# Optimization experiments

Measured on AMD Instinct MI355X. Metric: run time of the kernel, lower is better.

The kernel has to match this reference:

```python
import jax, jax.numpy as jnp
import numpy as np

H = 12          # number_of_heads
D = 768         # embedding_dim
DH = D // H     # head dim = 64
P = 14          # sqrt(num_patches) for image_size=224, patch=16
B, S = 64, 197  # batch, seq (196 patches + CLS)


def setup_inputs() -> dict:
    key = jax.random.key(0)
    ks = jax.random.split(key, 7)
    scale = 1.0 / np.sqrt(D)
    return {
        "q": jax.random.normal(ks[0], (B, S, D), jnp.float32),
        "k": jax.random.normal(ks[1], (B, S, D), jnp.float32),
        "v": jax.random.normal(ks[2], (B, S, D), jnp.float32),
        # nn.Linear weights, stored as [out, in]; applied as x @ W.T
        "Wq": jax.random.normal(ks[3], (D, D), jnp.float32) * scale,
        "Wk": jax.random.normal(ks[4], (D, D), jnp.float32) * scale,
        "Wv": jax.random.normal(ks[5], (D, D), jnp.float32) * scale,
        "Wo": jax.random.normal(ks[6], (D, D), jnp.float32) * scale,
    }


def reference(q, k, v, Wq, Wk, Wv, Wo):
    # Linear projections (bias=False): x @ W.T
    def proj(x, W):
        # [B,S,D] -> [B,H,S,DH]
        y = jnp.einsum('bsd,ed->bse', x, W)
        return y.reshape(B, S, H, DH).transpose(0, 2, 1, 3)

    qh, kh, vh = proj(q, Wq), proj(k, Wk), proj(v, Wv)

    # raw scores [B,H,S,S]
    scores = jnp.einsum('bhqd,bhkd->bhqk', qh, kh) / jnp.sqrt(jnp.asarray(DH, qh.dtype))
    attn = jax.nn.softmax(scores, axis=-1)

    # CLS (row 0) attention to the 196 patches -> [B,H,P,P]
    cls_to_patch_map = attn[:, :, 0, 1:].reshape(B, H, P, P)

    # dropout in eval mode (identity; deterministic reference)
    x = jnp.einsum('bhqk,bhkd->bhqd', attn, vh)          # [B,H,S,DH]
    x = x.transpose(0, 2, 1, 3).reshape(B, S, D)          # [B,S,D]
    output = jnp.einsum('bsd,ed->bse', x, Wo)
    return output, cls_to_patch_map
```

## Files before the change

### kernel.cpp

```cpp
#include <hip/hip_runtime.h>
#include <hip/hip_bf16.h>
#include <stdint.h>

#define DI __device__ __forceinline__

constexpr int Bn = 64;
constexpr int S  = 197;
constexpr int Dm = 768;
constexpr int H  = 12;
constexpr int DH = 64;
constexpr int M  = Bn * S;
constexpr int SP = 224;
constexpr int MD = M * Dm;
constexpr int WN = Dm * Dm;

typedef __attribute__((ext_vector_type(8))) short bf8;
typedef __attribute__((ext_vector_type(4))) float f4;

DI ushort f2bf(float f) {
  union { __hip_bfloat16 b; ushort u; } cv;
  cv.b = __float2bfloat16(f);
  return cv.u;
}

DI void gload_lds16(const void* g, const void* lds) {
  __builtin_amdgcn_global_load_lds(
      (__attribute__((address_space(1))) void*)(uintptr_t)g,
      (__attribute__((address_space(3))) void*)(uint32_t)(uintptr_t)lds,
      16, 0, 0);
}

DI bf8 ld16(const ushort* p) { return *(const bf8*)p; }

__global__ __launch_bounds__(256) void convert_all(
    const float4* __restrict__ q,  const float4* __restrict__ k,
    const float4* __restrict__ v,  const float4* __restrict__ wq,
    const float4* __restrict__ wk, const float4* __restrict__ wv,
    const float4* __restrict__ wo,
    ushort4* __restrict__ qb, ushort4* __restrict__ kb,
    ushort4* __restrict__ vb, ushort4* __restrict__ wb) {
  constexpr int NT = MD / 4;
  constexpr int NW = WN / 4;
  int i = blockIdx.x * 256 + threadIdx.x;
  const float4* src; ushort4* dst; int off;
  if (i < NT)            { src = q; dst = qb; off = i; }
  else if (i < 2 * NT)   { src = k; dst = kb; off = i - NT; }
  else if (i < 3 * NT)   { src = v; dst = vb; off = i - 2 * NT; }
  else {
    int j = i - 3 * NT;
    int wsel = j / NW; off = j - wsel * NW;
    src = wsel == 0 ? wq : wsel == 1 ? wk : wsel == 2 ? wv : wo;
    dst = wb + (size_t)wsel * NW;
  }
  float4 f = src[off];
  ushort4 u;
  u.x = f2bf(f.x); u.y = f2bf(f.y); u.z = f2bf(f.z); u.w = f2bf(f.w);
  dst[off] = u;
}


DI void stage128(const ushort* __restrict__ src, int rowmax, int row0,
                 int kcol0, ushort* lds, int w, int lane) {
#pragma unroll
  for (int l = 0; l < 2; ++l) {
    const int cid = w * 2 + l;
    const int c = cid * 64 + lane;
    const int rl = c >> 2;
    int rg = row0 + rl; if (rg > rowmax) rg = rowmax;
    const int k8 = (c & 3) ^ ((rl >> 1) & 3);
    gload_lds16(src + (size_t)rg * Dm + kcol0 + k8 * 8, lds + cid * 512);
  }
}

DI bf8 ldfrag(const ushort* buf, int row, int g) {
  return ld16(buf + row * 32 + ((g ^ ((row >> 1) & 3)) << 3));
}

#define KSTEP(KT, CUR, NXT)                                               \
  {                                                                       \
    if ((KT) < 23) {                                                      \
      stage128(A, M - 1, m0, ((KT) + 1) * 32, As[NXT], w, lane);          \
      stage128(W, 767, n0, ((KT) + 1) * 32, Bs[NXT], w, lane);            \
    }                                                                     \
    bf8 a[4], b[4];                                                       \
    _Pragma("unroll") for (int i = 0; i < 4; ++i)                         \
        a[i] = ldfrag(As[CUR], wr * 64 + i * 16 + rsel, g);               \
    _Pragma("unroll") for (int j = 0; j < 4; ++j)                         \
        b[j] = ldfrag(Bs[CUR], wc * 64 + j * 16 + rsel, g);               \
    __builtin_amdgcn_s_setprio(1);                                        \
    _Pragma("unroll") for (int i = 0; i < 4; ++i)                         \
      _Pragma("unroll") for (int j = 0; j < 4; ++j)                       \
        acc[i][j] = __builtin_amdgcn_mfma_f32_16x16x32_bf16(              \
            a[i], b[j], acc[i][j], 0, 0, 0);                              \
    __builtin_amdgcn_s_setprio(0);                                        \
    asm volatile("s_waitcnt vmcnt(0) lgkmcnt(0)" ::: "memory");           \
    __builtin_amdgcn_s_barrier();                                         \
  }

template <int MODE>
__global__ __launch_bounds__(256, 3) void gemmL(
    const ushort* __restrict__ Ab, const ushort* __restrict__ Wb,
    ushort* __restrict__ OQK, ushort* __restrict__ OV, float* __restrict__ OF) {
  __shared__ __align__(16) ushort As[2][128 * 32];
  __shared__ __align__(16) ushort Bs[2][128 * 32];
  constexpr int NT  = 6;
  constexpr int NWG = 594;
  const int tid = threadIdx.x, lane = tid & 63, w = tid >> 6;
  const int wr = w >> 1, wc = w & 1;
  const int rsel = lane & 15, g = lane >> 4;

  constexpr int qq = NWG / 8, rr = NWG % 8;
  const int bid = blockIdx.x;
  const int xcd = bid & 7, pos = bid >> 3;
  const int wg = (xcd < rr ? xcd * (qq + 1) : rr * (qq + 1) + (xcd - rr) * qq) + pos;
  const int nt = wg % NT, mt = wg / NT;
  const int n0 = nt * 128, m0 = mt * 128;
  const int z = blockIdx.y;
  const ushort* A = Ab + (size_t)z * MD;
  const ushort* W = Wb + (size_t)z * WN;

  const f4 fz = {0.f, 0.f, 0.f, 0.f};
  f4 acc[4][4];
#pragma unroll
  for (int i = 0; i < 4; i++)
#pragma unroll
    for (int j = 0; j < 4; j++) acc[i][j] = fz;

  stage128(A, M - 1, m0, 0, As[0], w, lane);
  stage128(W, 767, n0, 0, Bs[0], w, lane);
  asm volatile("s_waitcnt vmcnt(0)" ::: "memory");
  __builtin_amdgcn_s_barrier();

#pragma unroll 1
  for (int kt2 = 0; kt2 < 12; ++kt2) {
    const int kt = kt2 * 2;
    KSTEP(kt, 0, 1);
    KSTEP(kt + 1, 1, 0);
  }

#pragma unroll
  for (int i = 0; i < 4; i++) {
    const int mb = m0 + wr * 64 + i * 16 + g * 4;
#pragma unroll
    for (int j = 0; j < 4; j++) {
      const int n = n0 + wc * 64 + j * 16 + rsel;
#pragma unroll
      for (int rg = 0; rg < 4; rg++) {
        const int m = mb + rg;
        if (m < M) {
          const float val = acc[i][j][rg];
          if (MODE == 1) {
            OF[(size_t)m * Dm + n] = val;
          } else {
            const int b = m / S, s = m - b * S;
            const int hh = n >> 6, dh = n & 63;
            const ushort bv = f2bf(val);
            if (z < 2)
              OQK[(size_t)z * MD + (((size_t)b * H + hh) * S + s) * DH + dh] = bv;
            else
              OV[(((size_t)b * H + hh) * DH + dh) * SP + s] = bv;
          }
        }
      }
    }
  }
}

__global__ __launch_bounds__(256) void attn_fwd(
    const ushort* __restrict__ Qh, const ushort* __restrict__ Kh,
    const ushort* __restrict__ Vt, ushort* __restrict__ xh,
    float* __restrict__ outcls) {
  __shared__ __align__(16) ushort Pl[4][16][232];
  const int bh = blockIdx.x;
  const int b = bh / H, h = bh - b * H;
  const int tid = threadIdx.x, lane = tid & 63, w = tid >> 6;
  const int rsel = lane & 15, g = lane >> 4;
  const f4 fz = {0.f, 0.f, 0.f, 0.f};

#pragma unroll
  for (int t = 0; t < 6; t++) {
    int idx = t * 64 + lane;
    Pl[w][idx / 24][208 + idx % 24] = 0;
  }

  const ushort* Qs = Qh + (size_t)bh * S * DH;
  const ushort* Ks = Kh + (size_t)bh * S * DH;
  const ushort* Vs = Vt + (size_t)bh * DH * SP;

  for (int qt = w; qt < 13; qt += 4) {
    const int q0 = qt * 16;
    int qrow = q0 + rsel; if (qrow > S - 1) qrow = S - 1;
    const bf8 aq0 = ld16(Qs + qrow * DH + g * 8);
    const bf8 aq1 = ld16(Qs + qrow * DH + 32 + g * 8);

    f4 sc[13];
#pragma unroll
    for (int kt = 0; kt < 13; kt++) {
      int key = kt * 16 + rsel; if (key > S - 1) key = S - 1;
      const bf8 bk0 = ld16(Ks + key * DH + g * 8);
      const bf8 bk1 = ld16(Ks + key * DH + 32 + g * 8);
      f4 a = fz;
      a = __builtin_amdgcn_mfma_f32_16x16x32_bf16(aq0, bk0, a, 0, 0, 0);
      a = __builtin_amdgcn_mfma_f32_16x16x32_bf16(aq1, bk1, a, 0, 0, 0);
      sc[kt] = a * 0.125f;
    }

    float mx[4] = {-1e30f, -1e30f, -1e30f, -1e30f};
#pragma unroll
    for (int kt = 0; kt < 13; kt++) {
      const bool vmask = (kt * 16 + rsel) < S;
#pragma unroll
      for (int r = 0; r < 4; r++)
        if (vmask) mx[r] = fmaxf(mx[r], sc[kt][r]);
    }
#pragma unroll
    for (int d = 1; d < 16; d <<= 1)
#pragma unroll
      for (int r = 0; r < 4; r++) mx[r] = fmaxf(mx[r], __shfl_xor(mx[r], d));
    float sm[4] = {0.f, 0.f, 0.f, 0.f};
#pragma unroll
    for (int kt = 0; kt < 13; kt++) {
      const bool vmask = (kt * 16 + rsel) < S;
#pragma unroll
      for (int r = 0; r < 4; r++) {
        const float p = vmask ? exp2f((sc[kt][r] - mx[r]) * 1.44269504f) : 0.f;
        sc[kt][r] = p;
        sm[r] += p;
      }
    }
#pragma unroll
    for (int d = 1; d < 16; d <<= 1)
#pragma unroll
      for (int r = 0; r < 4; r++) sm[r] += __shfl_xor(sm[r], d);

    if (qt == 0 && g == 0) {
      const float inv0 = 1.f / sm[0];
#pragma unroll
      for (int kt = 0; kt < 13; kt++) {
        const int key = kt * 16 + rsel;
        if (key >= 1 && key < S)
          outcls[(size_t)bh * 196 + key - 1] = sc[kt][0] * inv0;
      }
    }

#pragma unroll
    for (int kt = 0; kt < 13; kt++)
#pragma unroll
      for (int r = 0; r < 4; r++)
        Pl[w][g * 4 + r][kt * 16 + rsel] = f2bf(sc[kt][r]);

    bf8 pa[7];
#pragma unroll
    for (int kc = 0; kc < 7; kc++)
      pa[kc] = ld16(&Pl[w][rsel][kc * 32 + g * 8]);
    float inv[4];
#pragma unroll
    for (int r = 0; r < 4; r++) inv[r] = 1.f / sm[r];
#pragma unroll
    for (int nt = 0; nt < 4; nt++) {
      f4 x = fz;
#pragma unroll
      for (int kc = 0; kc < 7; kc++) {
        const bf8 bv = ld16(Vs + (nt * 16 + rsel) * SP + kc * 32 + g * 8);
        x = __builtin_amdgcn_mfma_f32_16x16x32_bf16(pa[kc], bv, x, 0, 0, 0);
      }
#pragma unroll
      for (int r = 0; r < 4; r++) {
        const int s_ = q0 + g * 4 + r;
        if (s_ < S)
          xh[((size_t)b * S + s_) * Dm + h * DH + nt * 16 + rsel] = f2bf(x[r] * inv[r]);
      }
    }
  }
}

extern "C" void kernel_launch(void* const* d_in, const int* in_sizes, int n_in,
                              void* d_out, int out_size, void* d_ws, size_t ws_size,
                              hipStream_t stream) {
  (void)in_sizes; (void)n_in; (void)out_size; (void)ws_size;
  const float* q  = (const float*)d_in[0];
  const float* k  = (const float*)d_in[1];
  const float* v  = (const float*)d_in[2];
  const float* wq = (const float*)d_in[3];
  const float* wk = (const float*)d_in[4];
  const float* wv = (const float*)d_in[5];
  const float* wo = (const float*)d_in[6];

  uint8_t* ws = (uint8_t*)d_ws;
  ushort* qb = (ushort*)ws;
  ushort* kb = qb + (size_t)MD;
  ushort* vb = kb + (size_t)MD;
  ushort* wb = vb + (size_t)MD;
  ushort* Qh = wb + 4 * (size_t)WN;
  ushort* Kh = Qh + (size_t)MD;
  ushort* Vt = Kh + (size_t)MD;
  ushort* xh = qb;

  float* out    = (float*)d_out;
  float* outcls = out + (size_t)MD;

  hipMemsetAsync(Vt, 0, (size_t)Bn * H * DH * SP * sizeof(ushort), stream);

  constexpr int CONV_BLOCKS = (3 * (MD / 4) + 4 * (WN / 4)) / 256;
  convert_all<<<dim3(CONV_BLOCKS), 256, 0, stream>>>(
      (const float4*)q, (const float4*)k, (const float4*)v,
      (const float4*)wq, (const float4*)wk, (const float4*)wv, (const float4*)wo,
      (ushort4*)qb, (ushort4*)kb, (ushort4*)vb, (ushort4*)wb);

  gemmL<0><<<dim3(594, 3), 256, 0, stream>>>(qb, wb, Qh, Vt, nullptr);

  attn_fwd<<<dim3(Bn * H), 256, 0, stream>>>(Qh, Kh, Vt, xh, outcls);

  gemmL<1><<<dim3(594, 1), 256, 0, stream>>>(xh, wb + 3 * (size_t)WN, nullptr, nullptr, out);
}
```

Baseline: 318.5 us.

## Triple-buffer GEMM LDS staging with prefetch distance two

Replaces the double-buffered K loop in the projection GEMM with a three-stage LDS ring, issuing global-to-LDS loads two k-tiles ahead and waiting with a partial vmcnt instead of draining all loads each step. The aim is to hide global memory latency behind MFMA work. The s_setprio hints are removed. LDS use per block rises from 32KB to 48KB, which may limit occupancy under the 3-blocks-per-CU launch bound.

Result: no change. 319.2 us (+0.2%).

```diff
diff --git a/kernel.cpp b/kernel.cpp
--- a/kernel.cpp
+++ b/kernel.cpp
@@ -76,33 +76,12 @@
   return ld16(buf + row * 32 + ((g ^ ((row >> 1) & 3)) << 3));
 }
 
-#define KSTEP(KT, CUR, NXT)                                               \
-  {                                                                       \
-    if ((KT) < 23) {                                                      \
-      stage128(A, M - 1, m0, ((KT) + 1) * 32, As[NXT], w, lane);          \
-      stage128(W, 767, n0, ((KT) + 1) * 32, Bs[NXT], w, lane);            \
-    }                                                                     \
-    bf8 a[4], b[4];                                                       \
-    _Pragma("unroll") for (int i = 0; i < 4; ++i)                         \
-        a[i] = ldfrag(As[CUR], wr * 64 + i * 16 + rsel, g);               \
-    _Pragma("unroll") for (int j = 0; j < 4; ++j)                         \
-        b[j] = ldfrag(Bs[CUR], wc * 64 + j * 16 + rsel, g);               \
-    __builtin_amdgcn_s_setprio(1);                                        \
-    _Pragma("unroll") for (int i = 0; i < 4; ++i)                         \
-      _Pragma("unroll") for (int j = 0; j < 4; ++j)                       \
-        acc[i][j] = __builtin_amdgcn_mfma_f32_16x16x32_bf16(              \
-            a[i], b[j], acc[i][j], 0, 0, 0);                              \
-    __builtin_amdgcn_s_setprio(0);                                        \
-    asm volatile("s_waitcnt vmcnt(0) lgkmcnt(0)" ::: "memory");           \
-    __builtin_amdgcn_s_barrier();                                         \
-  }
-
 template <int MODE>
 __global__ __launch_bounds__(256, 3) void gemmL(
     const ushort* __restrict__ Ab, const ushort* __restrict__ Wb,
     ushort* __restrict__ OQK, ushort* __restrict__ OV, float* __restrict__ OF) {
-  __shared__ __align__(16) ushort As[2][128 * 32];
-  __shared__ __align__(16) ushort Bs[2][128 * 32];
+  __shared__ __align__(16) ushort As[3 * 128 * 32];
+  __shared__ __align__(16) ushort Bs[3 * 128 * 32];
   constexpr int NT  = 6;
   constexpr int NWG = 594;
   const int tid = threadIdx.x, lane = tid & 63, w = tid >> 6;
@@ -126,16 +105,38 @@
 #pragma unroll
     for (int j = 0; j < 4; j++) acc[i][j] = fz;
 
-  stage128(A, M - 1, m0, 0, As[0], w, lane);
-  stage128(W, 767, n0, 0, Bs[0], w, lane);
-  asm volatile("s_waitcnt vmcnt(0)" ::: "memory");
-  __builtin_amdgcn_s_barrier();
-
-#pragma unroll 1
-  for (int kt2 = 0; kt2 < 12; ++kt2) {
-    const int kt = kt2 * 2;
-    KSTEP(kt, 0, 1);
-    KSTEP(kt + 1, 1, 0);
+  stage128(A, M - 1, m0, 0,  As,        w, lane);
+  stage128(W, 767,   n0, 0,  Bs,        w, lane);
+  stage128(A, M - 1, m0, 32, As + 4096, w, lane);
+  stage128(W, 767,   n0, 32, Bs + 4096, w, lane);
+
+  int cb = 0;
+#pragma unroll 3
+  for (int kt = 0; kt < 24; ++kt) {
+    if (kt == 23) {
+      asm volatile("s_waitcnt vmcnt(0) lgkmcnt(0)" ::: "memory");
+    } else {
+      asm volatile("s_waitcnt vmcnt(4) lgkmcnt(0)" ::: "memory");
+    }
+    __builtin_amdgcn_s_barrier();
+    if (kt < 22) {
+      int pb = cb + 2; if (pb >= 3) pb -= 3;
+      stage128(A, M - 1, m0, (kt + 2) * 32, As + pb * 4096, w, lane);
+      stage128(W, 767,   n0, (kt + 2) * 32, Bs + pb * 4096, w, lane);
+    }
+    const ushort* cA = As + cb * 4096;
+    const ushort* cB = Bs + cb * 4096;
+    bf8 a[4], b[4];
+#pragma unroll
+    for (int i = 0; i < 4; ++i) a[i] = ldfrag(cA, wr * 64 + i * 16 + rsel, g);
+#pragma unroll
+    for (int j = 0; j < 4; ++j) b[j] = ldfrag(cB, wc * 64 + j * 16 + rsel, g);
+#pragma unroll
+    for (int i = 0; i < 4; ++i)
+#pragma unroll
+      for (int j = 0; j < 4; ++j)
+        acc[i][j] = __builtin_amdgcn_mfma_f32_16x16x32_bf16(a[i], b[j], acc[i][j], 0, 0, 0);
+    ++cb; if (cb == 3) cb = 0;
   }
 
 #pragma unroll
```

## Replace 128x128 GEMM with 256x256 8-wave tile and half-tile staged pipeline

Applied to the files above, without the earlier changes.

The projection GEMMs move from 128x128 tiles with 4 waves to 256x256 tiles with 8 waves. Each wave now holds a 128x64 accumulator block. The K loop now works on 64-wide tiles split into 32-wide halves over a 4-slot LDS ring, with vmcnt-gated barriers so global-to-LDS loads of later halves overlap the MFMA work. The aim is higher arithmetic intensity and fewer barrier stalls. In exchange the grid shrinks to 150 workgroups per z, which risks poorer CU utilisation and more padding waste at the M edge, and the kernel uses more registers and LDS.

Result: slower. 327.6 us (+2.8%).

```diff
diff --git a/kernel.cpp b/kernel.cpp
--- a/kernel.cpp
+++ b/kernel.cpp
@@ -59,88 +59,120 @@
 }
 
 
-DI void stage128(const ushort* __restrict__ src, int rowmax, int row0,
-                 int kcol0, ushort* lds, int w, int lane) {
+DI void stageH(const ushort* __restrict__ src, int rowmax, int row0,
+               int kcol0, ushort* lds, int w, int lane) {
 #pragma unroll
   for (int l = 0; l < 2; ++l) {
-    const int cid = w * 2 + l;
-    const int c = cid * 64 + lane;
-    const int rl = c >> 2;
+    const int cc = w * 2 + l;
+    const int rl = cc * 16 + (lane >> 2);
     int rg = row0 + rl; if (rg > rowmax) rg = rowmax;
-    const int k8 = (c & 3) ^ ((rl >> 1) & 3);
-    gload_lds16(src + (size_t)rg * Dm + kcol0 + k8 * 8, lds + cid * 512);
-  }
-}
-
-DI bf8 ldfrag(const ushort* buf, int row, int g) {
-  return ld16(buf + row * 32 + ((g ^ ((row >> 1) & 3)) << 3));
-}
-
-#define KSTEP(KT, CUR, NXT)                                               \
-  {                                                                       \
-    if ((KT) < 23) {                                                      \
-      stage128(A, M - 1, m0, ((KT) + 1) * 32, As[NXT], w, lane);          \
-      stage128(W, 767, n0, ((KT) + 1) * 32, Bs[NXT], w, lane);            \
-    }                                                                     \
-    bf8 a[4], b[4];                                                       \
-    _Pragma("unroll") for (int i = 0; i < 4; ++i)                         \
-        a[i] = ldfrag(As[CUR], wr * 64 + i * 16 + rsel, g);               \
-    _Pragma("unroll") for (int j = 0; j < 4; ++j)                         \
-        b[j] = ldfrag(Bs[CUR], wc * 64 + j * 16 + rsel, g);               \
-    __builtin_amdgcn_s_setprio(1);                                        \
-    _Pragma("unroll") for (int i = 0; i < 4; ++i)                         \
-      _Pragma("unroll") for (int j = 0; j < 4; ++j)                       \
-        acc[i][j] = __builtin_amdgcn_mfma_f32_16x16x32_bf16(              \
-            a[i], b[j], acc[i][j], 0, 0, 0);                              \
-    __builtin_amdgcn_s_setprio(0);                                        \
-    asm volatile("s_waitcnt vmcnt(0) lgkmcnt(0)" ::: "memory");           \
-    __builtin_amdgcn_s_barrier();                                         \
+    const int k8 = (lane & 3) ^ ((rl >> 1) & 3);
+    gload_lds16(src + (size_t)rg * Dm + kcol0 + k8 * 8, lds + cc * 512);
+  }
+}
+
+DI bf8 ldfragH(const ushort* half_, int row, int g) {
+  return ld16(half_ + row * 32 + ((g ^ ((row >> 1) & 3)) << 3));
+}
+
+#define GATE(NSTR) asm volatile("s_waitcnt vmcnt(" NSTR ")\ns_barrier" ::: "memory")
+
+#define TILE(T, SL, GA, GB, D01, D23)                                        \
+  {                                                                          \
+    const ushort* A0 = &As[SL][0][0]; const ushort* A1 = &As[SL][1][0];      \
+    const ushort* B0 = &Bs[SL][0][0]; const ushort* B1 = &Bs[SL][1][0];      \
+    bf8 a[4], b[4];                                                          \
+    GATE(GA);                                                                \
+    if (D01) stageH(Aa, M - 1, m0, (T)*64 + 96, &As[(SL)^1][1][0], w, lane); \
+    _Pragma("unroll") for (int j = 0; j < 4; ++j)                            \
+        b[j] = ldfragH(B0, wc * 64 + j * 16 + rsel, g);                      \
+    _Pragma("unroll") for (int i = 0; i < 4; ++i)                            \
+        a[i] = ldfragH(A0, wr * 128 + i * 16 + rsel, g);                     \
+    __builtin_amdgcn_s_setprio(1);                                           \
+    _Pragma("unroll") for (int i = 0; i < 4; ++i)                            \
+      _Pragma("unroll") for (int j = 0; j < 4; ++j)                          \
+        acc[i][j] = __builtin_amdgcn_mfma_f32_16x16x32_bf16(                 \
+            a[i], b[j], acc[i][j], 0, 0, 0);                                 \
+    __builtin_amdgcn_s_setprio(0);                                           \
+    if (D01) stageH(Ww, 767, n0, (T)*64 + 96, &Bs[(SL)^1][1][0], w, lane);   \
+    _Pragma("unroll") for (int i = 0; i < 4; ++i)                            \
+        a[i] = ldfragH(A0, wr * 128 + 64 + i * 16 + rsel, g);                \
+    __builtin_amdgcn_s_setprio(1);                                           \
+    _Pragma("unroll") for (int i = 0; i < 4; ++i)                            \
+      _Pragma("unroll") for (int j = 0; j < 4; ++j)                          \
+        acc[4 + i][j] = __builtin_amdgcn_mfma_f32_16x16x32_bf16(             \
+            a[i], b[j], acc[4 + i][j], 0, 0, 0);                             \
+    __builtin_amdgcn_s_setprio(0);                                           \
+    GATE(GB);                                                                \
+    if (D23) stageH(Aa, M - 1, m0, (T)*64 + 128, &As[SL][0][0], w, lane);    \
+    _Pragma("unroll") for (int j = 0; j < 4; ++j)                            \
+        b[j] = ldfragH(B1, wc * 64 + j * 16 + rsel, g);                      \
+    _Pragma("unroll") for (int i = 0; i < 4; ++i)                            \
+        a[i] = ldfragH(A1, wr * 128 + i * 16 + rsel, g);                     \
+    __builtin_amdgcn_s_setprio(1);                                           \
+    _Pragma("unroll") for (int i = 0; i < 4; ++i)                            \
+      _Pragma("unroll") for (int j = 0; j < 4; ++j)                          \
+        acc[i][j] = __builtin_amdgcn_mfma_f32_16x16x32_bf16(                 \
+            a[i], b[j], acc[i][j], 0, 0, 0);                                 \
+    __builtin_amdgcn_s_setprio(0);                                           \
+    if (D23) stageH(Ww, 767, n0, (T)*64 + 128, &Bs[SL][0][0], w, lane);      \
+    _Pragma("unroll") for (int i = 0; i < 4; ++i)                            \
+        a[i] = ldfragH(A1, wr * 128 + 64 + i * 16 + rsel, g);                \
+    __builtin_amdgcn_s_setprio(1);                                           \
+    _Pragma("unroll") for (int i = 0; i < 4; ++i)                            \
+      _Pragma("unroll") for (int j = 0; j < 4; ++j)                          \
+        acc[4 + i][j] = __builtin_amdgcn_mfma_f32_16x16x32_bf16(             \
+            a[i], b[j], acc[4 + i][j], 0, 0, 0);                             \
+    __builtin_amdgcn_s_setprio(0);                                           \
   }
 
 template <int MODE>
-__global__ __launch_bounds__(256, 3) void gemmL(
+__global__ __launch_bounds__(512, 2) void gemm8p(
     const ushort* __restrict__ Ab, const ushort* __restrict__ Wb,
     ushort* __restrict__ OQK, ushort* __restrict__ OV, float* __restrict__ OF) {
-  __shared__ __align__(16) ushort As[2][128 * 32];
-  __shared__ __align__(16) ushort Bs[2][128 * 32];
-  constexpr int NT  = 6;
-  constexpr int NWG = 594;
+  __shared__ __align__(16) ushort As[2][2][256 * 32];
+  __shared__ __align__(16) ushort Bs[2][2][256 * 32];
+  constexpr int NWG = 150;
   const int tid = threadIdx.x, lane = tid & 63, w = tid >> 6;
-  const int wr = w >> 1, wc = w & 1;
+  const int wr = w >> 2, wc = w & 3;
   const int rsel = lane & 15, g = lane >> 4;
 
   constexpr int qq = NWG / 8, rr = NWG % 8;
   const int bid = blockIdx.x;
   const int xcd = bid & 7, pos = bid >> 3;
   const int wg = (xcd < rr ? xcd * (qq + 1) : rr * (qq + 1) + (xcd - rr) * qq) + pos;
-  const int nt = wg % NT, mt = wg / NT;
-  const int n0 = nt * 128, m0 = mt * 128;
+  const int nt = wg % 3, mt = wg / 3;
+  const int n0 = nt * 256, m0 = mt * 256;
   const int z = blockIdx.y;
-  const ushort* A = Ab + (size_t)z * MD;
-  const ushort* W = Wb + (size_t)z * WN;
+  const ushort* Aa = Ab + (size_t)z * MD;
+  const ushort* Ww = Wb + (size_t)z * WN;
 
   const f4 fz = {0.f, 0.f, 0.f, 0.f};
-  f4 acc[4][4];
-#pragma unroll
-  for (int i = 0; i < 4; i++)
+  f4 acc[8][4];
+#pragma unroll
+  for (int i = 0; i < 8; i++)
 #pragma unroll
     for (int j = 0; j < 4; j++) acc[i][j] = fz;
 
-  stage128(A, M - 1, m0, 0, As[0], w, lane);
-  stage128(W, 767, n0, 0, Bs[0], w, lane);
-  asm volatile("s_waitcnt vmcnt(0)" ::: "memory");
-  __builtin_amdgcn_s_barrier();
+  stageH(Aa, M - 1, m0, 0,  &As[0][0][0], w, lane);
+  stageH(Ww, 767,   n0, 0,  &Bs[0][0][0], w, lane);
+  stageH(Aa, M - 1, m0, 32, &As[0][1][0], w, lane);
+  stageH(Ww, 767,   n0, 32, &Bs[0][1][0], w, lane);
+  stageH(Aa, M - 1, m0, 64, &As[1][0][0], w, lane);
+  stageH(Ww, 767,   n0, 64, &Bs[1][0][0], w, lane);
 
 #pragma unroll 1
-  for (int kt2 = 0; kt2 < 12; ++kt2) {
-    const int kt = kt2 * 2;
-    KSTEP(kt, 0, 1);
-    KSTEP(kt + 1, 1, 0);
-  }
-
-#pragma unroll
-  for (int i = 0; i < 4; i++) {
-    const int mb = m0 + wr * 64 + i * 16 + g * 4;
+  for (int tp = 0; tp < 5; ++tp) {
+    const int t0 = tp * 2;
+    TILE(t0,     0, "8", "8", 1, 1);
+    TILE(t0 + 1, 1, "8", "8", 1, 1);
+  }
+  TILE(10, 0, "8", "8", 1, 0);
+  TILE(11, 1, "4", "0", 0, 0);
+
+#pragma unroll
+  for (int i = 0; i < 8; i++) {
+    const int mb = m0 + wr * 128 + i * 16 + g * 4;
 #pragma unroll
     for (int j = 0; j < 4; j++) {
       const int n = n0 + wc * 64 + j * 16 + rsel;
@@ -307,9 +339,9 @@
       (const float4*)wq, (const float4*)wk, (const float4*)wv, (const float4*)wo,
       (ushort4*)qb, (ushort4*)kb, (ushort4*)vb, (ushort4*)wb);
 
-  gemmL<0><<<dim3(594, 3), 256, 0, stream>>>(qb, wb, Qh, Vt, nullptr);
+  gemm8p<0><<<dim3(150, 3), 512, 0, stream>>>(qb, wb, Qh, Vt, nullptr);
 
   attn_fwd<<<dim3(Bn * H), 256, 0, stream>>>(Qh, Kh, Vt, xh, outcls);
 
-  gemmL<1><<<dim3(594, 1), 256, 0, stream>>>(xh, wb + 3 * (size_t)WN, nullptr, nullptr, out);
-}
+  gemm8p<1><<<dim3(150, 1), 512, 0, stream>>>(xh, wb + 3 * (size_t)WN, nullptr, nullptr, out);
+}
```
